# Performance work log

Measured on AMD Instinct MI355X. Metric: run time of the kernel, lower is better.

Reference implementation:

```python
import jax, jax.numpy as jnp
import numpy as np

HV = 128          # hidden_value_dim
HT = 17           # hidden_type_dim
K = HT - 9        # number of per-type composition linears (8)
D = 2 * (HV + HT) # gate-linear input dim (290)
O = 5 * HV        # gate-linear output dim (640)
P = 400_000       # child-state pool size
N = 200_000       # number of parent compositions


def setup_inputs() -> dict:
    key = jax.random.key(0)
    ks = jax.random.split(key, 7)
    h_pool = jax.random.normal(ks[0], (P, HV), dtype=jnp.float32)
    c_pool = jax.random.normal(ks[1], (P, HV), dtype=jnp.float32)
    # soft type distributions per child (gumbel-softmax outputs in the original)
    t_pool = jax.random.uniform(ks[2], (P, HT), dtype=jnp.float32)
    child_idx = jax.random.randint(ks[3], (N, 2), 0, P)
    parent_type = jax.random.randint(ks[4], (N,), 0, K)
    # per-type composition weights (comp_linear_v), orthogonal-ish init -> plain normal scaled
    W = jax.random.normal(ks[5], (K, O, D), dtype=jnp.float32) / np.sqrt(D)
    b = jnp.zeros((K, O), dtype=jnp.float32)
    return {"h_pool": h_pool, "c_pool": c_pool, "t_pool": t_pool,
            "child_idx": child_idx, "parent_type": parent_type,
            "W": W, "b": b}


def _compose(h_pool, c_pool, t_pool, child_idx, parent_type, W, b):
    # gather children states  [N, hv] / [N, ht]
    li, ri = child_idx[:, 0], child_idx[:, 1]
    hl, hr = h_pool[li], h_pool[ri]
    cl, cr = c_pool[li], c_pool[ri]
    tl, tr = t_pool[li], t_pool[ri]
    # per-type linear input: concat(hl, tl, hr, tr)  [N, D]
    x = jnp.concatenate([hl, tl, hr, tr], axis=-1)
    # per-type gates via masked accumulation over the small fixed set of K types
    gates = jnp.zeros((x.shape[0], O), dtype=x.dtype)
    for k in range(K):
        yk = x @ W[k].T + b[k]                       # [N, O]
        gates = jnp.where((parent_type == k)[:, None], yk, gates)
    # binary tree-LSTM cell update: i, f_l, f_r, u, o
    i, fl, fr, u, o = jnp.split(gates, 5, axis=-1)
    c = (jax.nn.sigmoid(i) * jnp.tanh(u)
         + jax.nn.sigmoid(fl) * cl
         + jax.nn.sigmoid(fr) * cr)
    h = jax.nn.sigmoid(o) * jnp.tanh(c)
    return jnp.concatenate([h, c], axis=-1)         # [N, 2*hv]


def reference(h_pool, c_pool, t_pool, child_idx, parent_type, W, b):
    return _compose(h_pool, c_pool, t_pool, child_idx, parent_type, W, b)
```

## Files before the change

### kernel.cpp

```cpp
#include <hip/hip_runtime.h>
#include <hip/hip_bf16.h>

#define HV   128
#define HT   17
#define DIMD 290
#define KP   320
#define OO   640
#define RT   64
#define KN   8
#define NXCD 8

typedef unsigned short u16;
typedef __attribute__((ext_vector_type(8))) short short8v;
typedef __attribute__((ext_vector_type(4))) float f32x4;

__device__ __forceinline__ u16 f2bf(float x) {
    unsigned u = __float_as_uint(x);
    u = (u + 0x7FFFu + ((u >> 16) & 1u)) >> 16;
    return (u16)u;
}
__device__ __forceinline__ float sigf(float x) {
    return __builtin_amdgcn_rcpf(1.0f + __expf(-x));
}
__device__ __forceinline__ float tanhfast(float x) {
    return 1.0f - 2.0f * __builtin_amdgcn_rcpf(1.0f + __expf(2.0f * x));
}


__global__ void hist_k(const int* __restrict__ pt, int* __restrict__ hdr, int N) {
    __shared__ int c[KN];
    if (threadIdx.x < KN) c[threadIdx.x] = 0;
    __syncthreads();
    int n = blockIdx.x * 256 + threadIdx.x;
    if (n < N) atomicAdd(&c[pt[n]], 1);
    __syncthreads();
    if (threadIdx.x < KN && c[threadIdx.x]) atomicAdd(&hdr[threadIdx.x], c[threadIdx.x]);
}

__global__ void prefix_k(int* __restrict__ hdr) {
    if (threadIdx.x == 0 && blockIdx.x == 0) {
        int acc = 0;
        hdr[16] = 0;
        for (int k = 0; k < KN; ++k) {
            acc += (hdr[k] + RT - 1) / RT;
            hdr[17 + k] = acc;
        }
    }
}

__global__ void scatter_k(const int* __restrict__ pt, int* __restrict__ hdr,
                          int* __restrict__ idxbuf, int N) {
    __shared__ int c[KN], base[KN];
    if (threadIdx.x < KN) c[threadIdx.x] = 0;
    __syncthreads();
    int n = blockIdx.x * 256 + threadIdx.x;
    int k = 0, my = 0;
    if (n < N) { k = pt[n]; my = atomicAdd(&c[k], 1); }
    __syncthreads();
    if (threadIdx.x < KN)
        base[threadIdx.x] = c[threadIdx.x] ? atomicAdd(&hdr[8 + threadIdx.x], c[threadIdx.x]) : 0;
    __syncthreads();
    if (n < N) idxbuf[hdr[16 + k] * RT + base[k] + my] = n;
}

__global__ void wconv_k(const float* __restrict__ W, u16* __restrict__ Wt) {
    int k = blockIdx.y;
    int idx = blockIdx.x * 256 + threadIdx.x;
    if (idx >= OO * KP) return;
    int o = idx / KP, d = idx % KP;
    int src;
    if (d < 256)      src = (d < 128) ? d : d + 17;
    else if (d < 273) src = d - 128;
    else if (d < 290) src = d;
    else              src = -1;
    float v = (src >= 0) ? W[((size_t)k * OO + o) * DIMD + src] : 0.0f;
    int kk = d >> 5, e = d & 31;
    Wt[(((size_t)k * 10 + kk) * OO + o) * 32 + e] = f2bf(v);
}

__global__ __launch_bounds__(512, 2)
void fused_k(const float* __restrict__ h_pool, const float* __restrict__ c_pool,
             const float* __restrict__ t_pool, const int* __restrict__ child_idx,
             const float* __restrict__ bias, const u16* __restrict__ Wt,
             const int* __restrict__ hdr, const int* __restrict__ idxbuf,
             float* __restrict__ out) {
    __shared__ u16 sX[RT * KP];
    __shared__ int4 sMeta[2][RT];

    const int ntiles = hdr[24];

    const int nwg = gridDim.x;
    const int bq = nwg >> 3, br = nwg & (NXCD - 1);
    const int xcd = blockIdx.x & (NXCD - 1), ixc = blockIdx.x >> 3;
    const int sbid = (xcd < br ? xcd * (bq + 1) : br * (bq + 1) + (xcd - br) * bq) + ixc;

    const int t0 = sbid * 2;
    if (t0 >= ntiles) return;
    const int t1 = t0 + 1;
    const bool has1 = (t1 < ntiles);

    const int tid = threadIdx.x;
    const int r = tid >> 3, q = tid & 7;

    float4 A0[4], B0[4];
    float Tl0, Tl1, Tl2 = 0.f, Tr0, Tr1, Tr2 = 0.f;
    int sn, sl, sr2;

    auto loadmeta = [&](int tile) {
        sn = idxbuf[tile * RT + r];
        sl = 0; sr2 = 0;
        if (sn >= 0) { sl = child_idx[2 * sn]; sr2 = child_idx[2 * sn + 1]; }
    };
    auto issue_stage = [&]() {
        if (sn < 0) return;
        const float4* hl = (const float4*)(h_pool + (size_t)sl * HV);
        const float4* hr = (const float4*)(h_pool + (size_t)sr2 * HV);
        #pragma unroll
        for (int m = 0; m < 4; ++m) A0[m] = hl[q + 8 * m];
        #pragma unroll
        for (int m = 0; m < 4; ++m) B0[m] = hr[q + 8 * m];
        const float* tl = t_pool + (size_t)sl * HT;
        const float* tr = t_pool + (size_t)sr2 * HT;
        Tl0 = tl[q]; Tl1 = tl[q + 8];
        Tr0 = tr[q]; Tr1 = tr[q + 8];
        if (q == 0) { Tl2 = tl[16]; Tr2 = tr[16]; }
    };
    auto write_stage = [&]() {
        char* xr = (char*)sX + r * 640;
        const int swz = (r & 7) << 4;
        if (sn >= 0) {
            #pragma unroll
            for (int m = 0; m < 4; ++m) {
                float4 v = A0[m];
                *(ushort4*)(xr + (((q + 8 * m) * 8) ^ swz)) =
                    make_ushort4(f2bf(v.x), f2bf(v.y), f2bf(v.z), f2bf(v.w));
            }
            #pragma unroll
            for (int m = 0; m < 4; ++m) {
                float4 v = B0[m];
                *(ushort4*)(xr + ((256 + (q + 8 * m) * 8) ^ swz)) =
                    make_ushort4(f2bf(v.x), f2bf(v.y), f2bf(v.z), f2bf(v.w));
            }
            *(u16*)(xr + ((512 + 2 * q) ^ swz))       = f2bf(Tl0);
            *(u16*)(xr + ((512 + 2 * (q + 8)) ^ swz)) = f2bf(Tl1);
            *(u16*)(xr + ((546 + 2 * q) ^ swz))       = f2bf(Tr0);
            *(u16*)(xr + ((546 + 2 * (q + 8)) ^ swz)) = f2bf(Tr1);
            if (q == 0) {
                *(u16*)(xr + (544 ^ swz)) = f2bf(Tl2);
                *(u16*)(xr + (578 ^ swz)) = f2bf(Tr2);
            }
            for (int b = 580 + 2 * q; b < 640; b += 16)
                *(u16*)(xr + (b ^ swz)) = 0;
        } else {
            ushort4 z = make_ushort4(0, 0, 0, 0);
            for (int b = q * 8; b < 640; b += 64)
                *(ushort4*)(xr + (b ^ swz)) = z;
        }
    };

    loadmeta(t0);
    if (q == 0) sMeta[0][r] = make_int4(sn, sl, sr2, 0);
    issue_stage();
    write_stage();
    __syncthreads();

    const int wc = tid >> 6, lane = tid & 63;
    const int lo = lane & 15, hi = lane >> 4;
    const int hcol = wc * 16 + lo;
    const char* sXb = (const char*)sX;
    const int rowbase = lo * 640;
    const int swzl = (lo & 7) << 4;

    int k0 = 0;
    #pragma unroll
    for (int j = 0; j < 7; ++j) k0 += (t0 >= hdr[17 + j]);

    int wo[5];
    #pragma unroll
    for (int g = 0; g < 5; ++g)
        wo[g] = (g * 128 + hcol) * 32 + hi * 8;

    f32x4 acc[5][4];
    #pragma unroll
    for (int g = 0; g < 5; ++g)
        #pragma unroll
        for (int m = 0; m < 4; ++m)
            acc[g][m] = (f32x4){0.f, 0.f, 0.f, 0.f};

    {
        const u16* __restrict__ wt = Wt + ((size_t)k0 * 10 * OO) * 32;
        short8v wfA[5], wfB[5], wfC[5];
        #pragma unroll
        for (int g = 0; g < 5; ++g) wfA[g] = *(const short8v*)(wt + wo[g]);
        #pragma unroll
        for (int g = 0; g < 5; ++g) wfB[g] = *(const short8v*)(wt + (size_t)(OO * 32) + wo[g]);

        #pragma unroll
        for (int kk = 0; kk < 10; ++kk) {
            const int r3 = kk % 3;
            short8v (&wcur)[5] = (r3 == 0) ? wfA : (r3 == 1) ? wfB : wfC;
            short8v (&wnxt)[5] = (r3 == 0) ? wfC : (r3 == 1) ? wfA : wfB;
            if (kk < 8) {
                const u16* wtn = wt + (size_t)(kk + 2) * (OO * 32);
                #pragma unroll
                for (int g = 0; g < 5; ++g)
                    wnxt[g] = *(const short8v*)(wtn + wo[g]);
            }
            int a_off = rowbase + ((kk * 64 + hi * 16) ^ swzl);
            short8v a0 = *(const short8v*)(sXb + a_off);
            short8v a1 = *(const short8v*)(sXb + a_off + 10240);
            short8v a2 = *(const short8v*)(sXb + a_off + 20480);
            short8v a3 = *(const short8v*)(sXb + a_off + 30720);
            #pragma unroll
            for (int g = 0; g < 5; ++g) {
                acc[g][0] = __builtin_amdgcn_mfma_f32_16x16x32_bf16(a0, wcur[g], acc[g][0], 0, 0, 0);
                acc[g][1] = __builtin_amdgcn_mfma_f32_16x16x32_bf16(a1, wcur[g], acc[g][1], 0, 0, 0);
                acc[g][2] = __builtin_amdgcn_mfma_f32_16x16x32_bf16(a2, wcur[g], acc[g][2], 0, 0, 0);
                acc[g][3] = __builtin_amdgcn_mfma_f32_16x16x32_bf16(a3, wcur[g], acc[g][3], 0, 0, 0);
            }
        }
    }

    if (has1) {
        loadmeta(t1);
        if (q == 0) sMeta[1][r] = make_int4(sn, sl, sr2, 0);
        issue_stage();
    }
    __builtin_amdgcn_sched_barrier(0);

    float bb[5];
    #pragma unroll
    for (int g = 0; g < 5; ++g) bb[g] = bias[k0 * OO + g * 128 + hcol];

    int nodes[16];
    float cpl[16], cpr[16];
    #pragma unroll
    for (int m = 0; m < 4; ++m)
        #pragma unroll
        for (int jj = 0; jj < 4; ++jj) {
            int4 mt = sMeta[0][m * 16 + hi * 4 + jj];
            nodes[m * 4 + jj] = mt.x;
            cpl[m * 4 + jj] = c_pool[(size_t)mt.y * HV + hcol];
            cpr[m * 4 + jj] = c_pool[(size_t)mt.z * HV + hcol];
        }

    #pragma unroll
    for (int m = 0; m < 4; ++m) {
        #pragma unroll
        for (int jj = 0; jj < 4; ++jj) {
            int node = nodes[m * 4 + jj];
            if (node < 0) continue;
            float cl = cpl[m * 4 + jj], cr = cpr[m * 4 + jj];
            float gi  = acc[0][m][jj] + bb[0];
            float gfl = acc[1][m][jj] + bb[1];
            float gfr = acc[2][m][jj] + bb[2];
            float gu  = acc[3][m][jj] + bb[3];
            float go  = acc[4][m][jj] + bb[4];
            float cc = sigf(gi) * tanhfast(gu) + sigf(gfl) * cl + sigf(gfr) * cr;
            float hh = sigf(go) * tanhfast(cc);
            float* orow = out + (size_t)node * (2 * HV);
            orow[hcol]      = hh;
            orow[HV + hcol] = cc;
        }
    }

    if (!has1) return;

    __builtin_amdgcn_s_barrier();
    write_stage();
    asm volatile("s_waitcnt lgkmcnt(0)" ::: "memory");
    __builtin_amdgcn_s_barrier();

    int k1 = 0;
    #pragma unroll
    for (int j = 0; j < 7; ++j) k1 += (t1 >= hdr[17 + j]);

    #pragma unroll
    for (int g = 0; g < 5; ++g)
        #pragma unroll
        for (int m = 0; m < 4; ++m)
            acc[g][m] = (f32x4){0.f, 0.f, 0.f, 0.f};

    {
        const u16* __restrict__ wt = Wt + ((size_t)k1 * 10 * OO) * 32;
        short8v wfA[5], wfB[5], wfC[5];
        #pragma unroll
        for (int g = 0; g < 5; ++g) wfA[g] = *(const short8v*)(wt + wo[g]);
        #pragma unroll
        for (int g = 0; g < 5; ++g) wfB[g] = *(const short8v*)(wt + (size_t)(OO * 32) + wo[g]);

        #pragma unroll
        for (int kk = 0; kk < 10; ++kk) {
            const int r3 = kk % 3;
            short8v (&wcur)[5] = (r3 == 0) ? wfA : (r3 == 1) ? wfB : wfC;
            short8v (&wnxt)[5] = (r3 == 0) ? wfC : (r3 == 1) ? wfA : wfB;
            if (kk < 8) {
                const u16* wtn = wt + (size_t)(kk + 2) * (OO * 32);
                #pragma unroll
                for (int g = 0; g < 5; ++g)
                    wnxt[g] = *(const short8v*)(wtn + wo[g]);
            }
            int a_off = rowbase + ((kk * 64 + hi * 16) ^ swzl);
            short8v a0 = *(const short8v*)(sXb + a_off);
            short8v a1 = *(const short8v*)(sXb + a_off + 10240);
            short8v a2 = *(const short8v*)(sXb + a_off + 20480);
            short8v a3 = *(const short8v*)(sXb + a_off + 30720);
            #pragma unroll
            for (int g = 0; g < 5; ++g) {
                acc[g][0] = __builtin_amdgcn_mfma_f32_16x16x32_bf16(a0, wcur[g], acc[g][0], 0, 0, 0);
                acc[g][1] = __builtin_amdgcn_mfma_f32_16x16x32_bf16(a1, wcur[g], acc[g][1], 0, 0, 0);
                acc[g][2] = __builtin_amdgcn_mfma_f32_16x16x32_bf16(a2, wcur[g], acc[g][2], 0, 0, 0);
                acc[g][3] = __builtin_amdgcn_mfma_f32_16x16x32_bf16(a3, wcur[g], acc[g][3], 0, 0, 0);
            }
        }
    }

    #pragma unroll
    for (int g = 0; g < 5; ++g) bb[g] = bias[k1 * OO + g * 128 + hcol];

    #pragma unroll
    for (int m = 0; m < 4; ++m)
        #pragma unroll
        for (int jj = 0; jj < 4; ++jj) {
            int4 mt = sMeta[1][m * 16 + hi * 4 + jj];
            nodes[m * 4 + jj] = mt.x;
            cpl[m * 4 + jj] = c_pool[(size_t)mt.y * HV + hcol];
            cpr[m * 4 + jj] = c_pool[(size_t)mt.z * HV + hcol];
        }

    #pragma unroll
    for (int m = 0; m < 4; ++m) {
        #pragma unroll
        for (int jj = 0; jj < 4; ++jj) {
            int node = nodes[m * 4 + jj];
            if (node < 0) continue;
            float cl = cpl[m * 4 + jj], cr = cpr[m * 4 + jj];
            float gi  = acc[0][m][jj] + bb[0];
            float gfl = acc[1][m][jj] + bb[1];
            float gfr = acc[2][m][jj] + bb[2];
            float gu  = acc[3][m][jj] + bb[3];
            float go  = acc[4][m][jj] + bb[4];
            float cc = sigf(gi) * tanhfast(gu) + sigf(gfl) * cl + sigf(gfr) * cr;
            float hh = sigf(go) * tanhfast(cc);
            float* orow = out + (size_t)node * (2 * HV);
            orow[hcol]      = hh;
            orow[HV + hcol] = cc;
        }
    }
}

extern "C" void kernel_launch(void* const* d_in, const int* in_sizes, int n_in,
                              void* d_out, int out_size, void* d_ws, size_t ws_size,
                              hipStream_t stream) {
    const float* h_pool      = (const float*)d_in[0];
    const float* c_pool      = (const float*)d_in[1];
    const float* t_pool      = (const float*)d_in[2];
    const int*   child_idx   = (const int*)d_in[3];
    const int*   parent_type = (const int*)d_in[4];
    const float* W           = (const float*)d_in[5];
    const float* bias        = (const float*)d_in[6];
    float* out = (float*)d_out;

    const int N = in_sizes[3] / 2;
    const int maxblk = (N + RT - 1) / RT + KN;
    const int totrows = maxblk * RT;

    char* ws = (char*)d_ws;
    size_t off = 0;
    int* hdr = (int*)ws;                         off += 1024;
    int* idxbuf = (int*)(ws + off);              off += (((size_t)totrows * 4 + 255) / 256) * 256;
    u16* Wt = (u16*)(ws + off);                  off += (size_t)KN * OO * KP * 2;

    hipMemsetAsync(hdr, 0, 1024, stream);
    hipMemsetAsync(idxbuf, 0xFF, (size_t)totrows * 4, stream);

    int nb = (N + 255) / 256;
    hist_k<<<nb, 256, 0, stream>>>(parent_type, hdr, N);
    prefix_k<<<1, 64, 0, stream>>>(hdr);
    scatter_k<<<nb, 256, 0, stream>>>(parent_type, hdr, idxbuf, N);
    wconv_k<<<dim3((OO * KP + 255) / 256, KN), 256, 0, stream>>>(W, Wt);
    fused_k<<<(maxblk + 1) / 2, 512, 0, stream>>>(
        h_pool, c_pool, t_pool, child_idx, bias, Wt, hdr, idxbuf, out);
}
```

Baseline: 278.3 us.

## Overlap epilogue loads with tail MFMAs and prefetch next tile weights

Result: slower. 381.0 us (+36.9%).

```diff
diff --git a/kernel.cpp b/kernel.cpp
--- a/kernel.cpp
+++ b/kernel.cpp
@@ -20,10 +20,10 @@
     return (u16)u;
 }
 __device__ __forceinline__ float sigf(float x) {
-    return __builtin_amdgcn_rcpf(1.0f + __expf(-x));
+    return __builtin_amdgcn_rcpf(1.0f + exp2f(-1.44269504f * x));
 }
 __device__ __forceinline__ float tanhfast(float x) {
-    return 1.0f - 2.0f * __builtin_amdgcn_rcpf(1.0f + __expf(2.0f * x));
+    return 1.0f - 2.0f * __builtin_amdgcn_rcpf(1.0f + exp2f(2.88539008f * x));
 }
 
 
@@ -162,6 +162,10 @@
     if (q == 0) sMeta[0][r] = make_int4(sn, sl, sr2, 0);
     issue_stage();
     write_stage();
+    if (has1) {
+        loadmeta(t1);
+        if (q == 0) sMeta[1][r] = make_int4(sn, sl, sr2, 0);
+    }
     __syncthreads();
 
     const int wc = tid >> 6, lane = tid & 63;
@@ -171,9 +175,9 @@
     const int rowbase = lo * 640;
     const int swzl = (lo & 7) << 4;
 
-    int k0 = 0;
-    #pragma unroll
-    for (int j = 0; j < 7; ++j) k0 += (t0 >= hdr[17 + j]);
+    int k0 = 0, k1 = 0;
+    #pragma unroll
+    for (int j = 0; j < 7; ++j) { k0 += (t0 >= hdr[17 + j]); k1 += (t1 >= hdr[17 + j]); }
 
     int wo[5];
     #pragma unroll
@@ -187,20 +191,25 @@
         for (int m = 0; m < 4; ++m)
             acc[g][m] = (f32x4){0.f, 0.f, 0.f, 0.f};
 
+    int nodes[16];
+    float cpl[16], cpr[16];
+    float bb[5];
+    short8v wfA[5], wfB[5], wfC[5];
+    short8v wfA1[5], wfB1[5];
+
     {
         const u16* __restrict__ wt = Wt + ((size_t)k0 * 10 * OO) * 32;
-        short8v wfA[5], wfB[5], wfC[5];
         #pragma unroll
         for (int g = 0; g < 5; ++g) wfA[g] = *(const short8v*)(wt + wo[g]);
         #pragma unroll
         for (int g = 0; g < 5; ++g) wfB[g] = *(const short8v*)(wt + (size_t)(OO * 32) + wo[g]);
 
         #pragma unroll
-        for (int kk = 0; kk < 10; ++kk) {
+        for (int kk = 0; kk < 8; ++kk) {
             const int r3 = kk % 3;
             short8v (&wcur)[5] = (r3 == 0) ? wfA : (r3 == 1) ? wfB : wfC;
             short8v (&wnxt)[5] = (r3 == 0) ? wfC : (r3 == 1) ? wfA : wfB;
-            if (kk < 8) {
+            {
                 const u16* wtn = wt + (size_t)(kk + 2) * (OO * 32);
                 #pragma unroll
                 for (int g = 0; g < 5; ++g)
@@ -219,30 +228,51 @@
                 acc[g][3] = __builtin_amdgcn_mfma_f32_16x16x32_bf16(a3, wcur[g], acc[g][3], 0, 0, 0);
             }
         }
-    }
-
+
+        __builtin_amdgcn_sched_barrier(0);
+        #pragma unroll
+        for (int m = 0; m < 4; ++m)
+            #pragma unroll
+            for (int jj = 0; jj < 4; ++jj) {
+                int4 mt = sMeta[0][m * 16 + hi * 4 + jj];
+                nodes[m * 4 + jj] = mt.x;
+                cpl[m * 4 + jj] = c_pool[(size_t)mt.y * HV + hcol];
+                cpr[m * 4 + jj] = c_pool[(size_t)mt.z * HV + hcol];
+            }
+        #pragma unroll
+        for (int g = 0; g < 5; ++g) bb[g] = bias[k0 * OO + g * 128 + hcol];
+        __builtin_amdgcn_sched_barrier(0);
+
+        #pragma unroll
+        for (int kk = 8; kk < 10; ++kk) {
+            const int r3 = kk % 3;
+            short8v (&wcur)[5] = (r3 == 0) ? wfA : (r3 == 1) ? wfB : wfC;
+            int a_off = rowbase + ((kk * 64 + hi * 16) ^ swzl);
+            short8v a0 = *(const short8v*)(sXb + a_off);
+            short8v a1 = *(const short8v*)(sXb + a_off + 10240);
+            short8v a2 = *(const short8v*)(sXb + a_off + 20480);
+            short8v a3 = *(const short8v*)(sXb + a_off + 30720);
+            #pragma unroll
+            for (int g = 0; g < 5; ++g) {
+                acc[g][0] = __builtin_amdgcn_mfma_f32_16x16x32_bf16(a0, wcur[g], acc[g][0], 0, 0, 0);
+                acc[g][1] = __builtin_amdgcn_mfma_f32_16x16x32_bf16(a1, wcur[g], acc[g][1], 0, 0, 0);
+                acc[g][2] = __builtin_amdgcn_mfma_f32_16x16x32_bf16(a2, wcur[g], acc[g][2], 0, 0, 0);
+                acc[g][3] = __builtin_amdgcn_mfma_f32_16x16x32_bf16(a3, wcur[g], acc[g][3], 0, 0, 0);
+            }
+        }
+    }
+
+    __builtin_amdgcn_sched_barrier(0);
+    if (has1) issue_stage();
+    __builtin_amdgcn_sched_barrier(0);
     if (has1) {
-        loadmeta(t1);
-        if (q == 0) sMeta[1][r] = make_int4(sn, sl, sr2, 0);
-        issue_stage();
+        const u16* __restrict__ wt1 = Wt + ((size_t)k1 * 10 * OO) * 32;
+        #pragma unroll
+        for (int g = 0; g < 5; ++g) wfA1[g] = *(const short8v*)(wt1 + wo[g]);
+        #pragma unroll
+        for (int g = 0; g < 5; ++g) wfB1[g] = *(const short8v*)(wt1 + (size_t)(OO * 32) + wo[g]);
     }
     __builtin_amdgcn_sched_barrier(0);
-
-    float bb[5];
-    #pragma unroll
-    for (int g = 0; g < 5; ++g) bb[g] = bias[k0 * OO + g * 128 + hcol];
-
-    int nodes[16];
-    float cpl[16], cpr[16];
-    #pragma unroll
-    for (int m = 0; m < 4; ++m)
-        #pragma unroll
-        for (int jj = 0; jj < 4; ++jj) {
-            int4 mt = sMeta[0][m * 16 + hi * 4 + jj];
-            nodes[m * 4 + jj] = mt.x;
-            cpl[m * 4 + jj] = c_pool[(size_t)mt.y * HV + hcol];
-            cpr[m * 4 + jj] = c_pool[(size_t)mt.z * HV + hcol];
-        }
 
     #pragma unroll
     for (int m = 0; m < 4; ++m) {
@@ -271,10 +301,6 @@
     asm volatile("s_waitcnt lgkmcnt(0)" ::: "memory");
     __builtin_amdgcn_s_barrier();
 
-    int k1 = 0;
-    #pragma unroll
-    for (int j = 0; j < 7; ++j) k1 += (t1 >= hdr[17 + j]);
-
     #pragma unroll
     for (int g = 0; g < 5; ++g)
         #pragma unroll
@@ -283,18 +309,14 @@
 
     {
         const u16* __restrict__ wt = Wt + ((size_t)k1 * 10 * OO) * 32;
-        short8v wfA[5], wfB[5], wfC[5];
-        #pragma unroll
-        for (int g = 0; g < 5; ++g) wfA[g] = *(const short8v*)(wt + wo[g]);
-        #pragma unroll
-        for (int g = 0; g < 5; ++g) wfB[g] = *(const short8v*)(wt + (size_t)(OO * 32) + wo[g]);
-
-        #pragma unroll
-        for (int kk = 0; kk < 10; ++kk) {
+        short8v wfC1[5];
+
+        #pragma unroll
+        for (int kk = 0; kk < 8; ++kk) {
             const int r3 = kk % 3;
-            short8v (&wcur)[5] = (r3 == 0) ? wfA : (r3 == 1) ? wfB : wfC;
-            short8v (&wnxt)[5] = (r3 == 0) ? wfC : (r3 == 1) ? wfA : wfB;
-            if (kk < 8) {
+            short8v (&wcur)[5] = (r3 == 0) ? wfA1 : (r3 == 1) ? wfB1 : wfC1;
+            short8v (&wnxt)[5] = (r3 == 0) ? wfC1 : (r3 == 1) ? wfA1 : wfB1;
+            {
                 const u16* wtn = wt + (size_t)(kk + 2) * (OO * 32);
                 #pragma unroll
                 for (int g = 0; g < 5; ++g)
@@ -313,20 +335,39 @@
                 acc[g][3] = __builtin_amdgcn_mfma_f32_16x16x32_bf16(a3, wcur[g], acc[g][3], 0, 0, 0);
             }
         }
-    }
-
-    #pragma unroll
-    for (int g = 0; g < 5; ++g) bb[g] = bias[k1 * OO + g * 128 + hcol];
-
-    #pragma unroll
-    for (int m = 0; m < 4; ++m)
-        #pragma unroll
-        for (int jj = 0; jj < 4; ++jj) {
-            int4 mt = sMeta[1][m * 16 + hi * 4 + jj];
-            nodes[m * 4 + jj] = mt.x;
-            cpl[m * 4 + jj] = c_pool[(size_t)mt.y * HV + hcol];
-            cpr[m * 4 + jj] = c_pool[(size_t)mt.z * HV + hcol];
-        }
+
+        __builtin_amdgcn_sched_barrier(0);
+        #pragma unroll
+        for (int m = 0; m < 4; ++m)
+            #pragma unroll
+            for (int jj = 0; jj < 4; ++jj) {
+                int4 mt = sMeta[1][m * 16 + hi * 4 + jj];
+                nodes[m * 4 + jj] = mt.x;
+                cpl[m * 4 + jj] = c_pool[(size_t)mt.y * HV + hcol];
+                cpr[m * 4 + jj] = c_pool[(size_t)mt.z * HV + hcol];
+            }
+        #pragma unroll
+        for (int g = 0; g < 5; ++g) bb[g] = bias[k1 * OO + g * 128 + hcol];
+        __builtin_amdgcn_sched_barrier(0);
+
+        #pragma unroll
+        for (int kk = 8; kk < 10; ++kk) {
+            const int r3 = kk % 3;
+            short8v (&wcur)[5] = (r3 == 0) ? wfA1 : (r3 == 1) ? wfB1 : wfC1;
+            int a_off = rowbase + ((kk * 64 + hi * 16) ^ swzl);
+            short8v a0 = *(const short8v*)(sXb + a_off);
+            short8v a1 = *(const short8v*)(sXb + a_off + 10240);
+            short8v a2 = *(const short8v*)(sXb + a_off + 20480);
+            short8v a3 = *(const short8v*)(sXb + a_off + 30720);
+            #pragma unroll
+            for (int g = 0; g < 5; ++g) {
+                acc[g][0] = __builtin_amdgcn_mfma_f32_16x16x32_bf16(a0, wcur[g], acc[g][0], 0, 0, 0);
+                acc[g][1] = __builtin_amdgcn_mfma_f32_16x16x32_bf16(a1, wcur[g], acc[g][1], 0, 0, 0);
+                acc[g][2] = __builtin_amdgcn_mfma_f32_16x16x32_bf16(a2, wcur[g], acc[g][2], 0, 0, 0);
+                acc[g][3] = __builtin_amdgcn_mfma_f32_16x16x32_bf16(a3, wcur[g], acc[g][3], 0, 0, 0);
+            }
+        }
+    }
 
     #pragma unroll
     for (int m = 0; m < 4; ++m) {
```
